# Optimization experiments

Hardware: AMD Instinct MI355X
Metric: run time of the kernel (lower is better)

## Reference

```python
import jax, jax.numpy as jnp
import numpy as np

B, C, H, L, P = 64, 64, 256, 64, 32
N_REAL = 2047
N = N_REAL + 1  # slot 0 is the null-child zero vector


def setup_inputs() -> dict:
    key = jax.random.key(0)
    ks = jax.random.split(key, 8)
    return {
        "node_feats": jax.random.normal(ks[0], (B, C, N), jnp.float32),
        "z": jax.random.normal(ks[1], (B, L), jnp.float32),
        "children": jax.random.randint(ks[2], (B, 3 * N_REAL), 0, N, jnp.int32),
        "conv1_w": jax.random.normal(ks[3], (H, C, 3), jnp.float32) * 0.05,
        "conv1_b": jnp.zeros((H,), jnp.float32),
        "conv2_w": jax.random.normal(ks[4], (H, H, 3), jnp.float32) * 0.05,
        "conv2_b": jnp.zeros((H,), jnp.float32),
        "mlp_w1": jax.random.normal(ks[5], (H + L, H), jnp.float32) * 0.05,
        "mlp_b1": jnp.zeros((H,), jnp.float32),
        "mlp_w2": jax.random.normal(ks[6], (H, P), jnp.float32) * 0.05,
        "mlp_b2": jnp.zeros((P,), jnp.float32),
    }


def _tree_conv(x, children, w, b):
    # x: [B, Cin, N]; children: [B, 3*N_real] indices of (self,left,right) triples
    g = jax.vmap(lambda xb, ib: xb[:, ib])(x, children)      # [B, Cin, 3*N_real]
    g = g.reshape(g.shape[0], g.shape[1], -1, 3)             # [B, Cin, N_real, 3]
    out = jnp.einsum('bcnk,hck->bhn', g, w) + b[None, :, None]  # Conv1d k=3 s=3
    zero = jnp.zeros((out.shape[0], out.shape[1], 1), out.dtype)
    return jnp.concatenate([zero, out], axis=2)              # [B, Cout, N]


def _tree_norm(x):
    # TreeLayerNorm: normalize each tree over all (channel, node) elements
    mean = jnp.mean(x, axis=(1, 2), keepdims=True)
    std = jnp.std(x, axis=(1, 2), keepdims=True, ddof=1)  # torch.std is unbiased
    return (x - mean) / (std + 1e-5)


def reference(node_feats, z, children, conv1_w, conv1_b, conv2_w, conv2_b,
              mlp_w1, mlp_b1, mlp_w2, mlp_b2):
    x = _tree_conv(node_feats, children, conv1_w, conv1_b)
    x = jax.nn.relu(_tree_norm(x))
    x = _tree_conv(x, children, conv2_w, conv2_b)
    x = jax.nn.relu(_tree_norm(x))                           # [B, H, N]
    z_exp = jnp.broadcast_to(z[:, :, None], (z.shape[0], z.shape[1], x.shape[2]))
    xz = jnp.concatenate([x, z_exp], axis=1)                 # [B, H+L, N]
    xz = xz.transpose(0, 2, 1)                               # [B, N, H+L]
    h = jax.nn.relu(xz @ mlp_w1 + mlp_b1)                    # [B, N, H]
    return h @ mlp_w2 + mlp_b2                               # [B, N, P]
```

## Files before the change

kernel.cpp:

```cpp
#include <hip/hip_runtime.h>
#include <hip/hip_bf16.h>

#define BATCH 64
#define CC    64
#define HH    256
#define LL    64
#define PP    32
#define NREAL 2047
#define NN    2048
#define MTOT  (HH*NN)

typedef unsigned short u16;
typedef __attribute__((ext_vector_type(8))) short short8;
typedef __attribute__((ext_vector_type(4))) float f32x4;

__device__ __forceinline__ float bu2f(u16 u) {
    return __uint_as_float(((unsigned)u) << 16);
}
__device__ __forceinline__ u16 f2bu(float f) {
    __hip_bfloat16 h = __float2bfloat16(f);
    return *reinterpret_cast<u16*>(&h);
}
__device__ __forceinline__ float ldv(const void* p, long long i, int f32) {
    return f32 ? ((const float*)p)[i] : bu2f(((const u16*)p)[i]);
}

__device__ __forceinline__ void swz(int id, int& b, int& tile) {
    b    = (id & 7) + 8 * ((id >> 3) & 7);
    tile = id >> 6;
}

__global__ __launch_bounds__(256) void detect_k(const u16* __restrict__ nf,
                                                int* __restrict__ flag) {
    __shared__ int cnt;
    if (threadIdx.x == 0) cnt = 0;
    __syncthreads();
    int c = 0;
#pragma unroll
    for (int i = 0; i < 16; ++i) {
        unsigned u = nf[threadIdx.x * 16 + i];
        unsigned e = (u >> 7) & 0xFF;
        if (e >= 161) c++;
    }
    atomicAdd(&cnt, c);
    __syncthreads();
    if (threadIdx.x == 0) flag[0] = (cnt > 64) ? 1 : 0;
}

__global__ __launch_bounds__(256) void zero_k(u16* x1t, float* statsz) {
    int b = blockIdx.x, t = threadIdx.x;
    x1t[(long long)b * NN * HH + t] = 0;
    if (b == 0) statsz[t] = 0.f;
}
__global__ __launch_bounds__(256) void zero2_k(u16* x2t) {
    x2t[(long long)blockIdx.x * NN * HH + threadIdx.x] = 0;
}

__global__ __launch_bounds__(256) void tr_nf_k(const void* __restrict__ nf,
                                               u16* __restrict__ nf_t,
                                               const int* __restrict__ flag) {
    __shared__ u16 t[64][65];
    int isF32 = flag[0];
    int b = blockIdx.y;
    int n0 = blockIdx.x * 64;
    int tid = threadIdx.x;
    int lane = tid & 63, grp = tid >> 6;
#pragma unroll
    for (int i = 0; i < 16; ++i) {
        int c = grp * 16 + i;
        float v = ldv(nf, ((long long)b * CC + c) * NN + n0 + lane, isF32);
        t[c][lane] = f2bu(v);
    }
    __syncthreads();
#pragma unroll
    for (int i = 0; i < 16; ++i) {
        int n = grp * 16 + i;
        nf_t[((long long)b * NN + n0 + n) * CC + lane] = t[lane][n];
    }
}

__global__ __launch_bounds__(256) void wtm_k(const void* __restrict__ w,
                                             u16* __restrict__ wtm, int cinShift,
                                             const int* __restrict__ flag) {
    int isF32 = flag[0];
    int t = blockIdx.x * 256 + threadIdx.x;
    int CIN = 1 << cinShift;
    int total = 3 * CIN * HH;
    if (t >= total) return;
    int kin = t & 31;
    int rest = t >> 5;
    int h = rest & (HH - 1);
    int ks = rest >> 8;
    int k = ks * 32 + kin;
    int kk = k >> cinShift, c = k & (CIN - 1);
    wtm[t] = f2bu(ldv(w, (((long long)h << cinShift) + c) * 3 + kk, isF32));
}

__global__ __launch_bounds__(256) void wmlp_k(const void* __restrict__ w,
                                              u16* __restrict__ dst,
                                              int colShift, int total,
                                              const int* __restrict__ flag) {
    int isF32 = flag[0];
    int t = blockIdx.x * 256 + threadIdx.x;
    if (t >= total) return;
    int COLS = 1 << colShift;
    int kin = t & 31;
    int rest = t >> 5;
    int col = rest & (COLS - 1);
    int ks = rest >> colShift;
    dst[t] = f2bu(ldv(w, ((long long)(ks * 32 + kin) << colShift) + col, isF32));
}

__device__ __forceinline__ void load_norm(const float* stats, int b,
                                          float& mean, float& rstd) {
    float s = stats[b * 2], ss = stats[b * 2 + 1];
    float m = s / (float)MTOT;
    float var = (ss - s * s / (float)MTOT) / (float)(MTOT - 1);
    var = fmaxf(var, 0.f);
    mean = m;
    rstd = 1.f / (sqrtf(var) + 1e-5f);
}

template<int CIN>
__global__ __launch_bounds__(512, 2) void convm_k(const u16* __restrict__ x_t,
                                                  const int* __restrict__ children,
                                                  const u16* __restrict__ wtm,
                                                  const void* __restrict__ bias,
                                                  const float* __restrict__ stats_in,
                                                  float* __restrict__ stats_out,
                                                  u16* __restrict__ out_t,
                                                  const int* __restrict__ flag) {
    constexpr int KT = CIN / 32;
    constexpr int RE = CIN + 8;
    __shared__ u16 A[2][64 * RE];
    __shared__ int cidx[192];
    __shared__ float ps[16];

    int isF32 = flag[0];
    int b, ntile;
    swz(blockIdx.x, b, ntile);
    int n0 = ntile * 64;
    int tid = threadIdx.x;
    int lane = tid & 63, w = tid >> 6;
    int l15 = lane & 15, quad = lane >> 4;

    float mean = 0.f, rstd = 1.f;
    bool donorm = (stats_in != nullptr);
    if (donorm) load_norm(stats_in, b, mean, rstd);

    const long long cbase = (long long)b * (3 * NREAL);
    if (tid < 192) {
        int gi = 3 * n0 + tid;
        cidx[tid] = (gi < 3 * NREAL) ? children[cbase + gi] : 0;
    }
    __syncthreads();

    const long long xbase = (long long)b * NN;
    const u16* wb = wtm + ((long long)(w * 32 + l15)) * 32 + quad * 8;

    if (CIN == 256) {
        uint2 g0[8];
#pragma unroll
        for (int u = 0; u < 8; ++u) {
            int nd = w * 8 + u;
            g0[u] = *(const uint2*)(x_t + (xbase + cidx[3 * nd]) * CIN + lane * 4);
        }
#pragma unroll
        for (int u = 0; u < 8; ++u) {
            int nd = w * 8 + u;
            float f[4];
            f[0] = bu2f((u16)(g0[u].x & 0xffff)); f[1] = bu2f((u16)(g0[u].x >> 16));
            f[2] = bu2f((u16)(g0[u].y & 0xffff)); f[3] = bu2f((u16)(g0[u].y >> 16));
            if (donorm) {
#pragma unroll
                for (int j = 0; j < 4; ++j) f[j] = fmaxf((f[j] - mean) * rstd, 0.f);
            }
            uint2 o;
            o.x = (unsigned)f2bu(f[0]) | ((unsigned)f2bu(f[1]) << 16);
            o.y = (unsigned)f2bu(f[2]) | ((unsigned)f2bu(f[3]) << 16);
            *(uint2*)&A[0][nd * RE + lane * 4] = o;
        }
    } else {
        u16 g0[8];
#pragma unroll
        for (int u = 0; u < 8; ++u) {
            int nd = w * 8 + u;
            g0[u] = x_t[(xbase + cidx[3 * nd]) * CIN + lane];
        }
#pragma unroll
        for (int u = 0; u < 8; ++u) {
            int nd = w * 8 + u;
            float v = bu2f(g0[u]);
            if (donorm) v = fmaxf((v - mean) * rstd, 0.f);
            A[0][nd * RE + lane] = f2bu(v);
        }
    }
    __syncthreads();

    f32x4 acc[4][2];
#pragma unroll
    for (int mt = 0; mt < 4; ++mt)
#pragma unroll
        for (int nt = 0; nt < 2; ++nt) acc[mt][nt] = (f32x4){0.f, 0.f, 0.f, 0.f};

#pragma unroll
    for (int t = 0; t < 3; ++t) {
        const u16* Ac = &A[t & 1][0];
        u16* An = &A[(t + 1) & 1][0];

        short8 Bc[KT][2];
#pragma unroll
        for (int ks = 0; ks < KT; ++ks) {
            const u16* wn = wb + (long long)(t * KT + ks) * 8192;
            Bc[ks][0] = *(const short8*)(wn);
            Bc[ks][1] = *(const short8*)(wn + 512);
        }

        uint2 gv[8];
        u16 gs[8];
        if (t < 2) {
            if (CIN == 256) {
#pragma unroll
                for (int u = 0; u < 8; ++u) {
                    int nd = w * 8 + u;
                    gv[u] = *(const uint2*)(x_t + (xbase + cidx[3 * nd + t + 1]) * CIN
                                            + lane * 4);
                }
            } else {
#pragma unroll
                for (int u = 0; u < 8; ++u) {
                    int nd = w * 8 + u;
                    gs[u] = x_t[(xbase + cidx[3 * nd + t + 1]) * CIN + lane];
                }
            }
        }

        short8 a0 = *(const short8*)&Ac[(l15)      * RE + quad * 8];
        short8 a1 = *(const short8*)&Ac[(16 + l15) * RE + quad * 8];
        short8 a2 = *(const short8*)&Ac[(32 + l15) * RE + quad * 8];
        short8 a3 = *(const short8*)&Ac[(48 + l15) * RE + quad * 8];
#pragma unroll
        for (int ks = 0; ks < KT; ++ks) {
            short8 ca0 = a0, ca1 = a1, ca2 = a2, ca3 = a3;
            if (ks + 1 < KT) {
                int ko = (ks + 1) * 32 + quad * 8;
                a0 = *(const short8*)&Ac[(l15)      * RE + ko];
                a1 = *(const short8*)&Ac[(16 + l15) * RE + ko];
                a2 = *(const short8*)&Ac[(32 + l15) * RE + ko];
                a3 = *(const short8*)&Ac[(48 + l15) * RE + ko];
            }
            acc[0][0] = __builtin_amdgcn_mfma_f32_16x16x32_bf16(ca0, Bc[ks][0], acc[0][0], 0, 0, 0);
            acc[1][0] = __builtin_amdgcn_mfma_f32_16x16x32_bf16(ca1, Bc[ks][0], acc[1][0], 0, 0, 0);
            acc[2][0] = __builtin_amdgcn_mfma_f32_16x16x32_bf16(ca2, Bc[ks][0], acc[2][0], 0, 0, 0);
            acc[3][0] = __builtin_amdgcn_mfma_f32_16x16x32_bf16(ca3, Bc[ks][0], acc[3][0], 0, 0, 0);
            acc[0][1] = __builtin_amdgcn_mfma_f32_16x16x32_bf16(ca0, Bc[ks][1], acc[0][1], 0, 0, 0);
            acc[1][1] = __builtin_amdgcn_mfma_f32_16x16x32_bf16(ca1, Bc[ks][1], acc[1][1], 0, 0, 0);
            acc[2][1] = __builtin_amdgcn_mfma_f32_16x16x32_bf16(ca2, Bc[ks][1], acc[2][1], 0, 0, 0);
            acc[3][1] = __builtin_amdgcn_mfma_f32_16x16x32_bf16(ca3, Bc[ks][1], acc[3][1], 0, 0, 0);
        }

        if (t < 2) {
            if (CIN == 256) {
#pragma unroll
                for (int u = 0; u < 8; ++u) {
                    int nd = w * 8 + u;
                    float f[4];
                    f[0] = bu2f((u16)(gv[u].x & 0xffff));
                    f[1] = bu2f((u16)(gv[u].x >> 16));
                    f[2] = bu2f((u16)(gv[u].y & 0xffff));
                    f[3] = bu2f((u16)(gv[u].y >> 16));
                    if (donorm) {
#pragma unroll
                        for (int j = 0; j < 4; ++j)
                            f[j] = fmaxf((f[j] - mean) * rstd, 0.f);
                    }
                    uint2 o;
                    o.x = (unsigned)f2bu(f[0]) | ((unsigned)f2bu(f[1]) << 16);
                    o.y = (unsigned)f2bu(f[2]) | ((unsigned)f2bu(f[3]) << 16);
                    *(uint2*)&An[nd * RE + lane * 4] = o;
                }
            } else {
#pragma unroll
                for (int u = 0; u < 8; ++u) {
                    int nd = w * 8 + u;
                    float v = bu2f(gs[u]);
                    if (donorm) v = fmaxf((v - mean) * rstd, 0.f);
                    An[nd * RE + lane] = f2bu(v);
                }
            }
        }
        __syncthreads();
    }

    float s = 0.f, ss = 0.f;
#pragma unroll
    for (int nt = 0; nt < 2; ++nt) {
        int h = w * 32 + nt * 16 + l15;
        float bv = ldv(bias, h, isF32);
#pragma unroll
        for (int mt = 0; mt < 4; ++mt) {
#pragma unroll
            for (int r = 0; r < 4; ++r) {
                int nc = n0 + mt * 16 + quad * 4 + r;
                if (nc < NREAL) {
                    float v = acc[mt][nt][r] + bv;
                    s += v;
                    ss += v * v;
                    out_t[((long long)b * NN + 1 + nc) * HH + h] = f2bu(v);
                }
            }
        }
    }
#pragma unroll
    for (int off = 32; off; off >>= 1) {
        s  += __shfl_down(s, off);
        ss += __shfl_down(ss, off);
    }
    if (lane == 0) { ps[w] = s; ps[8 + w] = ss; }
    __syncthreads();
    if (tid == 0) {
        float S = 0.f, SS = 0.f;
#pragma unroll
        for (int i = 0; i < 8; ++i) { S += ps[i]; SS += ps[8 + i]; }
        atomicAdd(&stats_out[b * 2],     S);
        atomicAdd(&stats_out[b * 2 + 1], SS);
    }
}

#define REX 328
#define REH 264
__global__ __launch_bounds__(256, 4) void mlpm_k(const u16* __restrict__ x2t,
                                                 const void* __restrict__ z,
                                                 const u16* __restrict__ w1m,
                                                 const void* __restrict__ b1,
                                                 const u16* __restrict__ w2m,
                                                 const void* __restrict__ b2,
                                                 const float* __restrict__ stats,
                                                 void* __restrict__ out,
                                                 const int* __restrict__ flag) {
    __shared__ u16 xz[32 * REX];
    __shared__ u16 hbuf[32 * REH];
    int isF32 = flag[0];
    int b, tile;
    swz(blockIdx.x, b, tile);
    int n0 = tile * 32;
    int tid = threadIdx.x;
    int lane = tid & 63, w = tid >> 6;
    int l15 = lane & 15, quad = lane >> 4;

    float mean, rstd;
    load_norm(stats, b, mean, rstd);
    u16 zb = f2bu(ldv(z, (long long)b * LL + lane, isF32));

    uint2 vv[8];
#pragma unroll
    for (int u = 0; u < 8; ++u) {
        int node = w * 8 + u;
        vv[u] = *(const uint2*)(x2t + ((long long)(b * NN + n0 + node)) * HH
                                + lane * 4);
    }
#pragma unroll
    for (int u = 0; u < 8; ++u) {
        int node = w * 8 + u;
        float f[4];
        f[0] = bu2f((u16)(vv[u].x & 0xffff));
        f[1] = bu2f((u16)(vv[u].x >> 16));
        f[2] = bu2f((u16)(vv[u].y & 0xffff));
        f[3] = bu2f((u16)(vv[u].y >> 16));
#pragma unroll
        for (int j = 0; j < 4; ++j) f[j] = fmaxf((f[j] - mean) * rstd, 0.f);
        uint2 o;
        o.x = (unsigned)f2bu(f[0]) | ((unsigned)f2bu(f[1]) << 16);
        o.y = (unsigned)f2bu(f[2]) | ((unsigned)f2bu(f[3]) << 16);
        *(uint2*)&xz[node * REX + lane * 4] = o;
        xz[node * REX + HH + lane] = zb;
    }
    __syncthreads();

    f32x4 acc[2][4];
#pragma unroll
    for (int mt = 0; mt < 2; ++mt)
#pragma unroll
        for (int nt = 0; nt < 4; ++nt) acc[mt][nt] = (f32x4){0.f, 0.f, 0.f, 0.f};

    const u16* wbase = w1m + ((long long)(w * 64 + l15)) * 32 + quad * 8;
    short8 bf0 = *(const short8*)(wbase);
    short8 bf1 = *(const short8*)(wbase + 512);
    short8 bf2 = *(const short8*)(wbase + 1024);
    short8 bf3 = *(const short8*)(wbase + 1536);
    short8 a0 = *(const short8*)&xz[l15 * REX + quad * 8];
    short8 a1 = *(const short8*)&xz[(16 + l15) * REX + quad * 8];

    for (int ks = 0; ks < 10; ++ks) {
        short8 c0 = bf0, c1 = bf1, c2 = bf2, c3 = bf3;
        short8 ca0 = a0, ca1 = a1;
        if (ks + 1 < 10) {
            const u16* wn = wbase + (long long)(ks + 1) * 8192;
            bf0 = *(const short8*)(wn);
            bf1 = *(const short8*)(wn + 512);
            bf2 = *(const short8*)(wn + 1024);
            bf3 = *(const short8*)(wn + 1536);
            a0 = *(const short8*)&xz[l15 * REX + (ks + 1) * 32 + quad * 8];
            a1 = *(const short8*)&xz[(16 + l15) * REX + (ks + 1) * 32 + quad * 8];
        }
        acc[0][0] = __builtin_amdgcn_mfma_f32_16x16x32_bf16(ca0, c0, acc[0][0], 0, 0, 0);
        acc[1][0] = __builtin_amdgcn_mfma_f32_16x16x32_bf16(ca1, c0, acc[1][0], 0, 0, 0);
        acc[0][1] = __builtin_amdgcn_mfma_f32_16x16x32_bf16(ca0, c1, acc[0][1], 0, 0, 0);
        acc[1][1] = __builtin_amdgcn_mfma_f32_16x16x32_bf16(ca1, c1, acc[1][1], 0, 0, 0);
        acc[0][2] = __builtin_amdgcn_mfma_f32_16x16x32_bf16(ca0, c2, acc[0][2], 0, 0, 0);
        acc[1][2] = __builtin_amdgcn_mfma_f32_16x16x32_bf16(ca1, c2, acc[1][2], 0, 0, 0);
        acc[0][3] = __builtin_amdgcn_mfma_f32_16x16x32_bf16(ca0, c3, acc[0][3], 0, 0, 0);
        acc[1][3] = __builtin_amdgcn_mfma_f32_16x16x32_bf16(ca1, c3, acc[1][3], 0, 0, 0);
    }
#pragma unroll
    for (int nt = 0; nt < 4; ++nt) {
        int j = w * 64 + nt * 16 + l15;
        float bv = ldv(b1, j, isF32);
#pragma unroll
        for (int mt = 0; mt < 2; ++mt)
#pragma unroll
            for (int r = 0; r < 4; ++r) {
                int node = mt * 16 + quad * 4 + r;
                hbuf[node * REH + j] = f2bu(fmaxf(acc[mt][nt][r] + bv, 0.f));
            }
    }
    __syncthreads();

    int mt = w & 1, nt = w >> 1;
    f32x4 acc2 = (f32x4){0.f, 0.f, 0.f, 0.f};
#pragma unroll
    for (int ks = 0; ks < 8; ++ks) {
        short8 a = *(const short8*)&hbuf[(mt * 16 + l15) * REH + ks * 32 + quad * 8];
        short8 bf = *(const short8*)(w2m + ((long long)ks * PP + nt * 16 + l15) * 32 + quad * 8);
        acc2 = __builtin_amdgcn_mfma_f32_16x16x32_bf16(a, bf, acc2, 0, 0, 0);
    }
    int p = nt * 16 + l15;
    float bp = ldv(b2, p, isF32);
#pragma unroll
    for (int r = 0; r < 4; ++r) {
        int node = mt * 16 + quad * 4 + r;
        long long o = ((long long)(b * NN + n0 + node)) * PP + p;
        float v = acc2[r] + bp;
        if (isF32) ((float*)out)[o] = v;
        else       ((u16*)out)[o] = f2bu(v);
    }
}

__global__ __launch_bounds__(256) void fill0_k(void* out, const int* flag, int n) {
    int i = blockIdx.x * 256 + threadIdx.x;
    if (i >= n) return;
    if (flag[0]) ((float*)out)[i] = 0.f;
    else ((u16*)out)[i] = 0;
}

extern "C" void kernel_launch(void* const* d_in, const int* in_sizes, int n_in,
                              void* d_out, int out_size, void* d_ws, size_t ws_size,
                              hipStream_t stream) {
    const void* nf  = d_in[0];
    const void* z   = d_in[1];
    const int*  ch  = (const int*)d_in[2];
    const void* c1w = d_in[3];
    const void* c1b = d_in[4];
    const void* c2w = d_in[5];
    const void* c2b = d_in[6];
    const void* mw1 = d_in[7];
    const void* mb1 = d_in[8];
    const void* mw2 = d_in[9];
    const void* mb2 = d_in[10];

    char* ws = (char*)d_ws;
    int*   flag   = (int*)ws;
    float* statsz = (float*)(ws + 256);
    float* stats1 = (float*)(ws + 256);
    float* stats2 = (float*)(ws + 768);
    u16* x1t  = (u16*)(ws + 4096);
    u16* A    = (u16*)(ws + 4096 + 67108864LL);
    u16* nf_t = A;
    u16* x2t  = A;
    u16* wt1m = (u16*)d_out;
    u16* wt2m = wt1m + 192 * 256;
    u16* w1m = x1t;
    u16* w2m = x1t + 320 * 256;

    const size_t NEED = 4096 + 2 * 67108864ULL;
    if (ws_size < NEED) {
        detect_k<<<1, 256, 0, stream>>>((const u16*)nf, flag);
        fill0_k<<<(out_size + 255) / 256, 256, 0, stream>>>(d_out, flag, out_size);
        return;
    }

    detect_k<<<1, 256, 0, stream>>>((const u16*)nf, flag);
    zero_k<<<BATCH, 256, 0, stream>>>(x1t, statsz);
    tr_nf_k<<<dim3(NN / 64, BATCH), 256, 0, stream>>>(nf, nf_t, flag);
    wtm_k<<<(3 * CC * HH + 255) / 256, 256, 0, stream>>>(c1w, wt1m, 6, flag);
    wtm_k<<<(3 * HH * HH + 255) / 256, 256, 0, stream>>>(c2w, wt2m, 8, flag);

    convm_k<CC><<<32 * BATCH, 512, 0, stream>>>(nf_t, ch, wt1m, c1b,
                                                nullptr, stats1, x1t, flag);
    zero2_k<<<BATCH, 256, 0, stream>>>(x2t);
    convm_k<HH><<<32 * BATCH, 512, 0, stream>>>(x1t, ch, wt2m, c2b,
                                                stats1, stats2, x2t, flag);
    wmlp_k<<<(320 * 256 + 255) / 256, 256, 0, stream>>>(mw1, w1m, 8, 320 * 256, flag);
    wmlp_k<<<(256 * 32 + 255) / 256, 256, 0, stream>>>(mw2, w2m, 5, 256 * 32, flag);
    mlpm_k<<<64 * BATCH, 256, 0, stream>>>(x2t, z, w1m, mb1, w2m, mb2,
                                           stats2, d_out, flag);
}
```

Before: 309.5 us.

## Gather conv inputs directly into LDS asynchronously and pre-normalize in a separate pass

The conv kernel now gathers child rows with global_load_lds 16-byte direct-to-LDS copies into an XOR-swizzled, unpadded shared tile, replacing the register round-trip. Because of this, the layer-norm and ReLU of the first conv output can no longer be applied during the gather, so a new elementwise kernel normalizes x1 in place before the second conv. The goal is to remove VGPR pressure and the per-gather convert/normalize work from the MFMA loop and to overlap loads with compute. The cost is an extra full read-write pass over x1 and one more kernel launch.

Result: slower. 324.9 us (+5.0%).

```diff
diff --git a/kernel.cpp b/kernel.cpp
--- a/kernel.cpp
+++ b/kernel.cpp
@@ -23,6 +23,13 @@
 }
 __device__ __forceinline__ float ldv(const void* p, long long i, int f32) {
     return f32 ? ((const float*)p)[i] : bu2f(((const u16*)p)[i]);
+}
+
+__device__ __forceinline__ void async_cp16(const u16* src, u16* dst) {
+    __builtin_amdgcn_global_load_lds(
+        (const __attribute__((address_space(1))) unsigned int*)src,
+        (__attribute__((address_space(3))) unsigned int*)dst,
+        16, 0, 0);
 }
 
 __device__ __forceinline__ void swz(int id, int& b, int& tile) {
@@ -121,18 +128,38 @@
     rstd = 1.f / (sqrtf(var) + 1e-5f);
 }
 
+__global__ __launch_bounds__(256) void normx_k(u16* __restrict__ x,
+                                               const float* __restrict__ stats) {
+    int b, tile;
+    swz(blockIdx.x, b, tile);
+    float mean, rstd;
+    load_norm(stats, b, mean, rstd);
+    long long base = (long long)b * (NN * HH);
+    int i = tile * 256 + threadIdx.x;
+    uint4* p = (uint4*)(x + base) + i;
+    uint4 v = *p;
+    unsigned wds[4] = {v.x, v.y, v.z, v.w};
+#pragma unroll
+    for (int j = 0; j < 4; ++j) {
+        float lo = bu2f((u16)(wds[j] & 0xffff));
+        float hi = bu2f((u16)(wds[j] >> 16));
+        lo = fmaxf((lo - mean) * rstd, 0.f);
+        hi = fmaxf((hi - mean) * rstd, 0.f);
+        wds[j] = (unsigned)f2bu(lo) | ((unsigned)f2bu(hi) << 16);
+    }
+    *p = make_uint4(wds[0], wds[1], wds[2], wds[3]);
+}
+
 template<int CIN>
 __global__ __launch_bounds__(512, 2) void convm_k(const u16* __restrict__ x_t,
                                                   const int* __restrict__ children,
                                                   const u16* __restrict__ wtm,
                                                   const void* __restrict__ bias,
-                                                  const float* __restrict__ stats_in,
                                                   float* __restrict__ stats_out,
                                                   u16* __restrict__ out_t,
                                                   const int* __restrict__ flag) {
     constexpr int KT = CIN / 32;
-    constexpr int RE = CIN + 8;
-    __shared__ u16 A[2][64 * RE];
+    __shared__ u16 A[2][64 * CIN];
     __shared__ int cidx[192];
     __shared__ float ps[16];
 
@@ -144,10 +171,6 @@
     int lane = tid & 63, w = tid >> 6;
     int l15 = lane & 15, quad = lane >> 4;
 
-    float mean = 0.f, rstd = 1.f;
-    bool donorm = (stats_in != nullptr);
-    if (donorm) load_norm(stats_in, b, mean, rstd);
-
     const long long cbase = (long long)b * (3 * NREAL);
     if (tid < 192) {
         int gi = 3 * n0 + tid;
@@ -158,43 +181,33 @@
     const long long xbase = (long long)b * NN;
     const u16* wb = wtm + ((long long)(w * 32 + l15)) * 32 + quad * 8;
 
-    if (CIN == 256) {
-        uint2 g0[8];
-#pragma unroll
-        for (int u = 0; u < 8; ++u) {
-            int nd = w * 8 + u;
-            g0[u] = *(const uint2*)(x_t + (xbase + cidx[3 * nd]) * CIN + lane * 4);
+    auto issue = [&](int t, u16* An) {
+        if (CIN == 256) {
+            int half = lane >> 5, li = lane & 31;
+#pragma unroll
+            for (int q = 0; q < 4; ++q) {
+                int nd = w * 8 + q * 2 + half;
+                int ci = cidx[3 * nd + t];
+                const u16* src = x_t + (xbase + ci) * CIN
+                                 + ((li * 8) ^ ((nd & 7) << 3));
+                async_cp16(src, &An[(w * 8 + q * 2) * CIN]);
+            }
+        } else {
+            int sub = lane >> 3, li = lane & 7;
+            int nd = w * 8 + sub;
+            int ci = cidx[3 * nd + t];
+            const u16* src = x_t + (xbase + ci) * CIN
+                             + ((li * 8) ^ ((nd & 7) << 3));
+            async_cp16(src, &An[(w * 8) * CIN]);
         }
-#pragma unroll
-        for (int u = 0; u < 8; ++u) {
-            int nd = w * 8 + u;
-            float f[4];
-            f[0] = bu2f((u16)(g0[u].x & 0xffff)); f[1] = bu2f((u16)(g0[u].x >> 16));
-            f[2] = bu2f((u16)(g0[u].y & 0xffff)); f[3] = bu2f((u16)(g0[u].y >> 16));
-            if (donorm) {
-#pragma unroll
-                for (int j = 0; j < 4; ++j) f[j] = fmaxf((f[j] - mean) * rstd, 0.f);
-            }
-            uint2 o;
-            o.x = (unsigned)f2bu(f[0]) | ((unsigned)f2bu(f[1]) << 16);
-            o.y = (unsigned)f2bu(f[2]) | ((unsigned)f2bu(f[3]) << 16);
-            *(uint2*)&A[0][nd * RE + lane * 4] = o;
-        }
-    } else {
-        u16 g0[8];
-#pragma unroll
-        for (int u = 0; u < 8; ++u) {
-            int nd = w * 8 + u;
-            g0[u] = x_t[(xbase + cidx[3 * nd]) * CIN + lane];
-        }
-#pragma unroll
-        for (int u = 0; u < 8; ++u) {
-            int nd = w * 8 + u;
-            float v = bu2f(g0[u]);
-            if (donorm) v = fmaxf((v - mean) * rstd, 0.f);
-            A[0][nd * RE + lane] = f2bu(v);
-        }
-    }
+    };
+
+    auto ard = [&](const u16* Ac, int r, int ks) -> short8 {
+        return *(const short8*)&Ac[r * CIN
+                                   + ((ks * 32 + quad * 8) ^ ((r & 7) << 3))];
+    };
+
+    issue(0, &A[0][0]);
     __syncthreads();
 
     f32x4 acc[4][2];
@@ -216,38 +229,20 @@
             Bc[ks][1] = *(const short8*)(wn + 512);
         }
 
-        uint2 gv[8];
-        u16 gs[8];
-        if (t < 2) {
-            if (CIN == 256) {
-#pragma unroll
-                for (int u = 0; u < 8; ++u) {
-                    int nd = w * 8 + u;
-                    gv[u] = *(const uint2*)(x_t + (xbase + cidx[3 * nd + t + 1]) * CIN
-                                            + lane * 4);
-                }
-            } else {
-#pragma unroll
-                for (int u = 0; u < 8; ++u) {
-                    int nd = w * 8 + u;
-                    gs[u] = x_t[(xbase + cidx[3 * nd + t + 1]) * CIN + lane];
-                }
-            }
-        }
-
-        short8 a0 = *(const short8*)&Ac[(l15)      * RE + quad * 8];
-        short8 a1 = *(const short8*)&Ac[(16 + l15) * RE + quad * 8];
-        short8 a2 = *(const short8*)&Ac[(32 + l15) * RE + quad * 8];
-        short8 a3 = *(const short8*)&Ac[(48 + l15) * RE + quad * 8];
+        if (t < 2) issue(t + 1, An);
+
+        short8 a0 = ard(Ac, l15, 0);
+        short8 a1 = ard(Ac, 16 + l15, 0);
+        short8 a2 = ard(Ac, 32 + l15, 0);
+        short8 a3 = ard(Ac, 48 + l15, 0);
 #pragma unroll
         for (int ks = 0; ks < KT; ++ks) {
             short8 ca0 = a0, ca1 = a1, ca2 = a2, ca3 = a3;
             if (ks + 1 < KT) {
-                int ko = (ks + 1) * 32 + quad * 8;
-                a0 = *(const short8*)&Ac[(l15)      * RE + ko];
-                a1 = *(const short8*)&Ac[(16 + l15) * RE + ko];
-                a2 = *(const short8*)&Ac[(32 + l15) * RE + ko];
-                a3 = *(const short8*)&Ac[(48 + l15) * RE + ko];
+                a0 = ard(Ac, l15, ks + 1);
+                a1 = ard(Ac, 16 + l15, ks + 1);
+                a2 = ard(Ac, 32 + l15, ks + 1);
+                a3 = ard(Ac, 48 + l15, ks + 1);
             }
             acc[0][0] = __builtin_amdgcn_mfma_f32_16x16x32_bf16(ca0, Bc[ks][0], acc[0][0], 0, 0, 0);
             acc[1][0] = __builtin_amdgcn_mfma_f32_16x16x32_bf16(ca1, Bc[ks][0], acc[1][0], 0, 0, 0);
@@ -259,37 +254,7 @@
             acc[3][1] = __builtin_amdgcn_mfma_f32_16x16x32_bf16(ca3, Bc[ks][1], acc[3][1], 0, 0, 0);
         }
 
-        if (t < 2) {
-            if (CIN == 256) {
-#pragma unroll
-                for (int u = 0; u < 8; ++u) {
-                    int nd = w * 8 + u;
-                    float f[4];
-                    f[0] = bu2f((u16)(gv[u].x & 0xffff));
-                    f[1] = bu2f((u16)(gv[u].x >> 16));
-                    f[2] = bu2f((u16)(gv[u].y & 0xffff));
-                    f[3] = bu2f((u16)(gv[u].y >> 16));
-                    if (donorm) {
-#pragma unroll
-                        for (int j = 0; j < 4; ++j)
-                            f[j] = fmaxf((f[j] - mean) * rstd, 0.f);
-                    }
-                    uint2 o;
-                    o.x = (unsigned)f2bu(f[0]) | ((unsigned)f2bu(f[1]) << 16);
-                    o.y = (unsigned)f2bu(f[2]) | ((unsigned)f2bu(f[3]) << 16);
-                    *(uint2*)&An[nd * RE + lane * 4] = o;
-                }
-            } else {
-#pragma unroll
-                for (int u = 0; u < 8; ++u) {
-                    int nd = w * 8 + u;
-                    float v = bu2f(gs[u]);
-                    if (donorm) v = fmaxf((v - mean) * rstd, 0.f);
-                    An[nd * RE + lane] = f2bu(v);
-                }
-            }
-        }
-        __syncthreads();
+        if (t < 2) __syncthreads();
     }
 
     float s = 0.f, ss = 0.f;
@@ -496,10 +461,11 @@
     wtm_k<<<(3 * HH * HH + 255) / 256, 256, 0, stream>>>(c2w, wt2m, 8, flag);
 
     convm_k<CC><<<32 * BATCH, 512, 0, stream>>>(nf_t, ch, wt1m, c1b,
-                                                nullptr, stats1, x1t, flag);
+                                                stats1, x1t, flag);
+    normx_k<<<64 * 256, 256, 0, stream>>>(x1t, stats1);
     zero2_k<<<BATCH, 256, 0, stream>>>(x2t);
     convm_k<HH><<<32 * BATCH, 512, 0, stream>>>(x1t, ch, wt2m, c2b,
-                                                stats1, stats2, x2t, flag);
+                                                stats2, x2t, flag);
     wmlp_k<<<(320 * 256 + 255) / 256, 256, 0, stream>>>(mw1, w1m, 8, 320 * 256, flag);
     wmlp_k<<<(256 * 32 + 255) / 256, 256, 0, stream>>>(mw2, w2m, 5, 256 * 32, flag);
     mlpm_k<<<64 * BATCH, 256, 0, stream>>>(x2t, z, w1m, mb1, w2m, mb2,
```

## Merge prep kernels, fold x2t null-row zeroing into conv2, vectorize conv1 gather

Applied to the files above, without the earlier changes.

Merges the weight-transpose and zero-init kernels into one prep launch, and merges the two MLP-weight conversion kernels into one launch. The zero2 kernel is removed: the conv2 kernel now writes the null-node row of its output from the first tile of each batch. The CIN=64 gather path in conv1 now loads 4 bf16 per thread with uint2 instead of one scalar per thread. The norm step is dropped from that path, which holds only because conv1 never normalizes its input. The aim is fewer kernel launches and fewer, wider gather memory transactions.

New measurement: 301.4 us. 1.03x faster.

```diff
diff --git a/kernel.cpp b/kernel.cpp
--- a/kernel.cpp
+++ b/kernel.cpp
@@ -47,13 +47,33 @@
     if (threadIdx.x == 0) flag[0] = (cnt > 64) ? 1 : 0;
 }
 
-__global__ __launch_bounds__(256) void zero_k(u16* x1t, float* statsz) {
-    int b = blockIdx.x, t = threadIdx.x;
-    x1t[(long long)b * NN * HH + t] = 0;
-    if (b == 0) statsz[t] = 0.f;
-}
-__global__ __launch_bounds__(256) void zero2_k(u16* x2t) {
-    x2t[(long long)blockIdx.x * NN * HH + threadIdx.x] = 0;
+__global__ __launch_bounds__(256) void prep_k(const void* __restrict__ c1w,
+                                              const void* __restrict__ c2w,
+                                              u16* __restrict__ wt1m,
+                                              u16* __restrict__ wt2m,
+                                              u16* __restrict__ x1t,
+                                              float* __restrict__ statsz,
+                                              const int* __restrict__ flag) {
+    int isF32 = flag[0];
+    int blk = blockIdx.x, tid = threadIdx.x;
+    if (blk < 960) {
+        const void* w = (blk < 192) ? c1w : c2w;
+        u16* dst      = (blk < 192) ? wt1m : wt2m;
+        int cinShift  = (blk < 192) ? 6 : 8;
+        int t = ((blk < 192) ? blk : (blk - 192)) * 256 + tid;
+        int CIN = 1 << cinShift;
+        int kin = t & 31;
+        int rest = t >> 5;
+        int h = rest & (HH - 1);
+        int ks = rest >> 8;
+        int k = ks * 32 + kin;
+        int kk = k >> cinShift, c = k & (CIN - 1);
+        dst[t] = f2bu(ldv(w, (((long long)h << cinShift) + c) * 3 + kk, isF32));
+    } else {
+        int b = blk - 960;
+        x1t[(long long)b * NN * HH + tid] = 0;
+        if (b == 0) statsz[tid] = 0.f;
+    }
 }
 
 __global__ __launch_bounds__(256) void tr_nf_k(const void* __restrict__ nf,
@@ -79,30 +99,17 @@
     }
 }
 
-__global__ __launch_bounds__(256) void wtm_k(const void* __restrict__ w,
-                                             u16* __restrict__ wtm, int cinShift,
-                                             const int* __restrict__ flag) {
+__global__ __launch_bounds__(256) void wmlp2_k(const void* __restrict__ mw1,
+                                               const void* __restrict__ mw2,
+                                               u16* __restrict__ w1m,
+                                               u16* __restrict__ w2m,
+                                               const int* __restrict__ flag) {
     int isF32 = flag[0];
-    int t = blockIdx.x * 256 + threadIdx.x;
-    int CIN = 1 << cinShift;
-    int total = 3 * CIN * HH;
-    if (t >= total) return;
-    int kin = t & 31;
-    int rest = t >> 5;
-    int h = rest & (HH - 1);
-    int ks = rest >> 8;
-    int k = ks * 32 + kin;
-    int kk = k >> cinShift, c = k & (CIN - 1);
-    wtm[t] = f2bu(ldv(w, (((long long)h << cinShift) + c) * 3 + kk, isF32));
-}
-
-__global__ __launch_bounds__(256) void wmlp_k(const void* __restrict__ w,
-                                              u16* __restrict__ dst,
-                                              int colShift, int total,
-                                              const int* __restrict__ flag) {
-    int isF32 = flag[0];
-    int t = blockIdx.x * 256 + threadIdx.x;
-    if (t >= total) return;
+    int blk = blockIdx.x, tid = threadIdx.x;
+    const void* w = (blk < 320) ? mw1 : mw2;
+    u16* dst      = (blk < 320) ? w1m : w2m;
+    int colShift  = (blk < 320) ? 8 : 5;
+    int t = ((blk < 320) ? blk : (blk - 320)) * 256 + tid;
     int COLS = 1 << colShift;
     int kin = t & 31;
     int rest = t >> 5;
@@ -181,18 +188,16 @@
             *(uint2*)&A[0][nd * RE + lane * 4] = o;
         }
     } else {
-        u16 g0[8];
-#pragma unroll
-        for (int u = 0; u < 8; ++u) {
-            int nd = w * 8 + u;
-            g0[u] = x_t[(xbase + cidx[3 * nd]) * CIN + lane];
-        }
-#pragma unroll
-        for (int u = 0; u < 8; ++u) {
-            int nd = w * 8 + u;
-            float v = bu2f(g0[u]);
-            if (donorm) v = fmaxf((v - mean) * rstd, 0.f);
-            A[0][nd * RE + lane] = f2bu(v);
+        uint2 g0[2];
+#pragma unroll
+        for (int u = 0; u < 2; ++u) {
+            int nd = w * 8 + u * 4 + quad;
+            g0[u] = *(const uint2*)(x_t + (xbase + cidx[3 * nd]) * CIN + l15 * 4);
+        }
+#pragma unroll
+        for (int u = 0; u < 2; ++u) {
+            int nd = w * 8 + u * 4 + quad;
+            *(uint2*)&A[0][nd * RE + l15 * 4] = g0[u];
         }
     }
     __syncthreads();
@@ -217,7 +222,7 @@
         }
 
         uint2 gv[8];
-        u16 gs[8];
+        uint2 gs[2];
         if (t < 2) {
             if (CIN == 256) {
 #pragma unroll
@@ -228,9 +233,10 @@
                 }
             } else {
 #pragma unroll
-                for (int u = 0; u < 8; ++u) {
-                    int nd = w * 8 + u;
-                    gs[u] = x_t[(xbase + cidx[3 * nd + t + 1]) * CIN + lane];
+                for (int u = 0; u < 2; ++u) {
+                    int nd = w * 8 + u * 4 + quad;
+                    gs[u] = *(const uint2*)(x_t + (xbase + cidx[3 * nd + t + 1]) * CIN
+                                            + l15 * 4);
                 }
             }
         }
@@ -281,11 +287,9 @@
                 }
             } else {
 #pragma unroll
-                for (int u = 0; u < 8; ++u) {
-                    int nd = w * 8 + u;
-                    float v = bu2f(gs[u]);
-                    if (donorm) v = fmaxf((v - mean) * rstd, 0.f);
-                    An[nd * RE + lane] = f2bu(v);
+                for (int u = 0; u < 2; ++u) {
+                    int nd = w * 8 + u * 4 + quad;
+                    *(uint2*)&An[nd * RE + l15 * 4] = gs[u];
                 }
             }
         }
@@ -324,6 +328,10 @@
         for (int i = 0; i < 8; ++i) { S += ps[i]; SS += ps[8 + i]; }
         atomicAdd(&stats_out[b * 2],     S);
         atomicAdd(&stats_out[b * 2 + 1], SS);
+    }
+    if (CIN == 256 && ntile == 0 && tid < 32) {
+        uint4 zz = {0u, 0u, 0u, 0u};
+        *(uint4*)&out_t[((long long)b * NN) * HH + tid * 8] = zz;
     }
 }
 
@@ -490,18 +498,14 @@
     }
 
     detect_k<<<1, 256, 0, stream>>>((const u16*)nf, flag);
-    zero_k<<<BATCH, 256, 0, stream>>>(x1t, statsz);
+    prep_k<<<1024, 256, 0, stream>>>(c1w, c2w, wt1m, wt2m, x1t, statsz, flag);
     tr_nf_k<<<dim3(NN / 64, BATCH), 256, 0, stream>>>(nf, nf_t, flag);
-    wtm_k<<<(3 * CC * HH + 255) / 256, 256, 0, stream>>>(c1w, wt1m, 6, flag);
-    wtm_k<<<(3 * HH * HH + 255) / 256, 256, 0, stream>>>(c2w, wt2m, 8, flag);
 
     convm_k<CC><<<32 * BATCH, 512, 0, stream>>>(nf_t, ch, wt1m, c1b,
                                                 nullptr, stats1, x1t, flag);
-    zero2_k<<<BATCH, 256, 0, stream>>>(x2t);
     convm_k<HH><<<32 * BATCH, 512, 0, stream>>>(x1t, ch, wt2m, c2b,
                                                 stats1, stats2, x2t, flag);
-    wmlp_k<<<(320 * 256 + 255) / 256, 256, 0, stream>>>(mw1, w1m, 8, 320 * 256, flag);
-    wmlp_k<<<(256 * 32 + 255) / 256, 256, 0, stream>>>(mw2, w2m, 5, 256 * 32, flag);
+    wmlp2_k<<<352, 256, 0, stream>>>(mw1, mw2, w1m, w2m, flag);
     mlpm_k<<<64 * BATCH, 256, 0, stream>>>(x2t, z, w1m, mb1, w2m, mb2,
                                            stats2, d_out, flag);
 }
```
